# Optimization experiments

Hardware: AMD Instinct MI355X
Metric: run time of the kernel (lower is better)

The kernel has to match this reference:

```python
import jax, jax.numpy as jnp
import numpy as np

IN_F = 4096
OUT_F = 4096
RANK = 16
NUM_SLOTS = 32
ALPHA = 1.0


def setup_inputs() -> dict:
    key = jax.random.key(0)
    k_x, k_w, k_b, k_a, k_bm, k_idx = jax.random.split(key, 6)
    x = jax.random.normal(k_x, (8, 2048, IN_F), dtype=jnp.float32)
    weight = jax.random.normal(k_w, (OUT_F, IN_F), dtype=jnp.float32) * (1.0 / np.sqrt(IN_F))
    bias = jax.random.normal(k_b, (OUT_F,), dtype=jnp.float32) * 0.01
    lora_A = jax.random.normal(k_a, (NUM_SLOTS, IN_F, RANK), dtype=jnp.float32) * 1e-4
    lora_B = jax.random.normal(k_bm, (NUM_SLOTS, RANK, OUT_F), dtype=jnp.float32) * 1e-4
    lora_indices = jax.random.randint(k_idx, (8,), 0, NUM_SLOTS)
    return {"x": x, "weight": weight, "bias": bias, "lora_A": lora_A,
            "lora_B": lora_B, "lora_indices": lora_indices}


def reference(x, weight, bias, lora_A, lora_B, lora_indices):
    # base linear: x @ W.T + b
    out = jnp.einsum('bsd,od->bso', x, weight) + bias
    # per-sample LoRA slot gather + low-rank bmm chain
    chosen_A = lora_A[lora_indices]          # [B, in, r]
    chosen_B = lora_B[lora_indices]          # [B, r, out]
    inter = jnp.einsum('bsd,bdr->bsr', x, chosen_A)       # [B, S, r]
    out_lora = jnp.einsum('bsr,bro->bso', inter, chosen_B)  # [B, S, out]
    return out + ALPHA * out_lora
```

## Files before the change

### kernel.cpp

```cpp
#include <hip/hip_runtime.h>
#include <hip/hip_bf16.h>


#define M_TOT 16384
#define K_TOT 4096
#define N_TOT 4096
#define RANK 16
#define NT2 64

typedef __attribute__((ext_vector_type(8))) short bf16x8;
typedef __attribute__((ext_vector_type(4))) float f32x4;
typedef __attribute__((ext_vector_type(16))) float f32x16;

__device__ __forceinline__ unsigned short f2bf(float f) {
  unsigned int u = __builtin_bit_cast(unsigned int, f);
  u += 0x7fffu + ((u >> 16) & 1u);
  return (unsigned short)(u >> 16);
}

__global__ void cvt_bf16_kernel(const float* __restrict__ src,
                                unsigned short* __restrict__ dst, int n4) {
  int i = blockIdx.x * blockDim.x + threadIdx.x;
  const int stride = gridDim.x * blockDim.x;
  for (; i < n4; i += stride) {
    const float4 v = reinterpret_cast<const float4*>(src)[i];
    ushort4 o;
    o.x = f2bf(v.x); o.y = f2bf(v.y); o.z = f2bf(v.z); o.w = f2bf(v.w);
    reinterpret_cast<ushort4*>(dst)[i] = o;
  }
}

__global__ __launch_bounds__(256) void lora_inter_mfma_kernel(
    const unsigned short* __restrict__ xb,
    const float* __restrict__ loraA,
    const int* __restrict__ idx,
    float* __restrict__ inter) {
  const int lane = threadIdx.x & 63;
  const int wv = threadIdx.x >> 6;
  const int m0 = blockIdx.x * 64 + wv * 16;
  const int slot = idx[m0 >> 11];
  const int q = lane >> 4;
  const int c = lane & 15;
  const unsigned short* __restrict__ xrow = xb + (size_t)(m0 + c) * K_TOT + q * 8;
  const float* __restrict__ Abase = loraA + (size_t)slot * K_TOT * RANK + c;

  f32x4 acc = (f32x4){0.f, 0.f, 0.f, 0.f};
#pragma unroll 4
  for (int kt = 0; kt < K_TOT; kt += 32) {
    const bf16x8 af = *reinterpret_cast<const bf16x8*>(xrow + kt);
    const float* __restrict__ Ak = Abase + (size_t)(kt + q * 8) * RANK;
    bf16x8 bfr;
#pragma unroll
    for (int j = 0; j < 8; ++j) bfr[j] = (short)f2bf(Ak[(size_t)j * RANK]);
    acc = __builtin_amdgcn_mfma_f32_16x16x32_bf16(af, bfr, acc, 0, 0, 0);
  }
#pragma unroll
  for (int i = 0; i < 4; ++i)
    inter[(size_t)(m0 + q * 4 + i) * RANK + c] = acc[i];
}

__device__ __forceinline__ void gload16(const void* g, void* l) {
  __builtin_amdgcn_global_load_lds(
      (const __attribute__((address_space(1))) unsigned int*)g,
      (__attribute__((address_space(3))) unsigned int*)l, 16, 0, 0);
}

#define GBARRIER() asm volatile("s_barrier" ::: "memory")
#define RD(p) (*reinterpret_cast<const bf16x8*>(p))

__global__ __launch_bounds__(512, 2) void gemm_fused_kernel(
    const unsigned short* __restrict__ xb,
    const unsigned short* __restrict__ wb,
    const float* __restrict__ bias,
    const float* __restrict__ inter,
    const float* __restrict__ loraB,
    const int* __restrict__ idx,
    float* __restrict__ out) {
  __shared__ unsigned short lds[2][32768];
  char* ldsB = (char*)&lds[0][0];

  const int tid = threadIdx.x;
  const int lane = tid & 63;
  const int wv = tid >> 6;
  const int wr = wv >> 2;
  const int wc = wv & 3;

  const int bid = ((blockIdx.x & 7) << 7) | (blockIdx.x >> 3);
  const int m0 = (bid >> 4) << 8;
  const int n0 = (bid & 15) << 8;

  const int r0 = tid >> 3;
  const int scol = ((tid & 7) ^ (r0 & 7) ^ (((r0 >> 4) & 1) << 2)) << 3;
  const unsigned short* xsrc = xb + (size_t)(m0 + r0) * K_TOT + scol;
  const unsigned short* wsrc = wb + (size_t)(n0 + r0) * K_TOT + scol;
  const int stg = tid << 4;

#define STAGE64(t)                                                       \
  do {                                                                   \
    const int _bo = (((t) & 1) << 16);                                   \
    const size_t _ko = (size_t)(t) * 64;                                 \
    gload16(xsrc + _ko,                        ldsB + _bo + stg);        \
    gload16(xsrc + (size_t)64  * K_TOT + _ko,  ldsB + _bo + 8192 + stg); \
    gload16(xsrc + (size_t)128 * K_TOT + _ko,  ldsB + _bo + 16384 + stg);\
    gload16(xsrc + (size_t)192 * K_TOT + _ko,  ldsB + _bo + 24576 + stg);\
    gload16(wsrc + _ko,                        ldsB + _bo + 32768 + stg);\
    gload16(wsrc + (size_t)64  * K_TOT + _ko,  ldsB + _bo + 40960 + stg);\
    gload16(wsrc + (size_t)128 * K_TOT + _ko,  ldsB + _bo + 49152 + stg);\
    gload16(wsrc + (size_t)192 * K_TOT + _ko,  ldsB + _bo + 57344 + stg);\
  } while (0)

  const int rowl = lane & 31;
  const int hc = (((lane >> 5) ^ (lane & 7) ^ (((lane >> 4) & 1) << 2)) << 4);
  const int abase = (wr * 128 + rowl) * 128 + hc;
  const int bbase = 32768 + (wc * 64 + rowl) * 128 + hc;

  f32x16 acc[4][2];
#pragma unroll
  for (int i = 0; i < 4; ++i)
#pragma unroll
    for (int j = 0; j < 2; ++j)
#pragma unroll
      for (int e = 0; e < 16; ++e) acc[i][j][e] = 0.f;

  STAGE64(0);
  asm volatile("s_waitcnt vmcnt(0)" ::: "memory");
  GBARRIER();

#pragma unroll 1
  for (int t = 0; t < NT2; ++t) {
    const char* base = ldsB + ((t & 1) << 16);
    bf16x8 af[8], bf0[4], bf1[4];

#pragma unroll
    for (int ni = 0; ni < 2; ++ni)
#pragma unroll
      for (int kk = 0; kk < 2; ++kk)
        bf0[ni * 2 + kk] = RD(base + ((bbase + ni * 4096) ^ (kk << 5)));
#pragma unroll
    for (int mi = 0; mi < 4; ++mi)
#pragma unroll
      for (int kk = 0; kk < 2; ++kk)
        af[mi * 2 + kk] = RD(base + ((abase + mi * 4096) ^ (kk << 5)));
#pragma unroll
    for (int ni = 0; ni < 2; ++ni)
#pragma unroll
      for (int kk = 0; kk < 2; ++kk)
        bf1[ni * 2 + kk] = RD(base + ((bbase + ni * 4096) ^ ((2 + kk) << 5)));
    if (t < NT2 - 1) STAGE64(t + 1);

    asm volatile("s_waitcnt lgkmcnt(4)" ::: "memory");
    __builtin_amdgcn_sched_barrier(0);
    __builtin_amdgcn_s_setprio(1);
#pragma unroll
    for (int mi = 0; mi < 4; ++mi)
#pragma unroll
      for (int ni = 0; ni < 2; ++ni)
#pragma unroll
        for (int kk = 0; kk < 2; ++kk)
          acc[mi][ni] = __builtin_amdgcn_mfma_f32_32x32x16_bf16(
              af[mi * 2 + kk], bf0[ni * 2 + kk], acc[mi][ni], 0, 0, 0);
    __builtin_amdgcn_s_setprio(0);
    __builtin_amdgcn_sched_barrier(0);

#pragma unroll
    for (int mi = 0; mi < 4; ++mi)
#pragma unroll
      for (int kk = 0; kk < 2; ++kk)
        af[mi * 2 + kk] = RD(base + ((abase + mi * 4096) ^ ((2 + kk) << 5)));
    asm volatile("s_waitcnt lgkmcnt(0)" ::: "memory");
    __builtin_amdgcn_sched_barrier(0);
    __builtin_amdgcn_s_setprio(1);
#pragma unroll
    for (int mi = 0; mi < 4; ++mi)
#pragma unroll
      for (int ni = 0; ni < 2; ++ni)
#pragma unroll
        for (int kk = 0; kk < 2; ++kk)
          acc[mi][ni] = __builtin_amdgcn_mfma_f32_32x32x16_bf16(
              af[mi * 2 + kk], bf1[ni * 2 + kk], acc[mi][ni], 0, 0, 0);
    __builtin_amdgcn_s_setprio(0);
    __builtin_amdgcn_sched_barrier(0);

    asm volatile("s_waitcnt vmcnt(0)" ::: "memory");
    GBARRIER();
  }

  const int slot = idx[m0 >> 11];
  const float* __restrict__ Bmat = loraB + (size_t)slot * RANK * N_TOT;
  const int halfsel = (lane >> 5) << 2;
  const int gn0 = n0 + wc * 64 + rowl;

  float bcv[2][RANK];
  float bv[2];
#pragma unroll
  for (int ni = 0; ni < 2; ++ni) {
    const int gn = gn0 + ni * 32;
    bv[ni] = bias[gn];
#pragma unroll
    for (int p = 0; p < RANK; ++p) bcv[ni][p] = Bmat[(size_t)p * N_TOT + gn];
  }
#pragma unroll
  for (int mi = 0; mi < 4; ++mi) {
#pragma unroll
    for (int r = 0; r < 16; ++r) {
      const int gm = m0 + wr * 128 + mi * 32 + (r & 3) + 8 * (r >> 2) + halfsel;
      const float4* ivp = reinterpret_cast<const float4*>(inter + (size_t)gm * RANK);
      const float4 iv0 = ivp[0], iv1 = ivp[1], iv2 = ivp[2], iv3 = ivp[3];
      float* orow = out + (size_t)gm * N_TOT;
#pragma unroll
      for (int ni = 0; ni < 2; ++ni) {
        const float lora =
            iv0.x * bcv[ni][0]  + iv0.y * bcv[ni][1]  + iv0.z * bcv[ni][2]  + iv0.w * bcv[ni][3] +
            iv1.x * bcv[ni][4]  + iv1.y * bcv[ni][5]  + iv1.z * bcv[ni][6]  + iv1.w * bcv[ni][7] +
            iv2.x * bcv[ni][8]  + iv2.y * bcv[ni][9]  + iv2.z * bcv[ni][10] + iv2.w * bcv[ni][11] +
            iv3.x * bcv[ni][12] + iv3.y * bcv[ni][13] + iv3.z * bcv[ni][14] + iv3.w * bcv[ni][15];
        orow[gn0 + ni * 32] = acc[mi][ni][r] + bv[ni] + lora;
      }
    }
  }
#undef STAGE64
}

extern "C" void kernel_launch(void* const* d_in, const int* in_sizes, int n_in,
                              void* d_out, int out_size, void* d_ws, size_t ws_size,
                              hipStream_t stream) {
  const float* x     = (const float*)d_in[0];
  const float* w     = (const float*)d_in[1];
  const float* bias  = (const float*)d_in[2];
  const float* loraA = (const float*)d_in[3];
  const float* loraB = (const float*)d_in[4];
  const int*   idx   = (const int*)d_in[5];
  float* out = (float*)d_out;

  char* ws = (char*)d_ws;
  unsigned short* xb   = (unsigned short*)ws;
  unsigned short* wbuf = (unsigned short*)(ws + 134217728);
  float* inter = (float*)(ws + 134217728 + 33554432);

  cvt_bf16_kernel<<<2048, 256, 0, stream>>>(x, xb, M_TOT * K_TOT / 4);
  cvt_bf16_kernel<<<1024, 256, 0, stream>>>(w, wbuf, N_TOT * K_TOT / 4);
  lora_inter_mfma_kernel<<<M_TOT / 64, 256, 0, stream>>>(xb, loraA, idx, inter);
  gemm_fused_kernel<<<(M_TOT / 256) * (N_TOT / 256), 512, 0, stream>>>(
      xb, wbuf, bias, inter, loraB, idx, out);
}
```

Measured before the change: 718.9 us.

## Stage GEMM tiles in MFMA fragment order to make LDS reads linear

Reorganizes how global-to-LDS staging assigns rows and k-chunks so that each wavefront's 16-byte LDS slot already holds the fragment an MFMA lane needs. Fragment reads then become linear lane-contiguous addresses instead of XOR-swizzled ones, which removes swizzle arithmetic and aims at conflict-free ds_reads. The catch is that global loads become less coalesced: each lane fetches a 16-byte piece from a different row, and each thread now keeps eight separate source pointers in registers.

```diff
diff --git a/kernel.cpp b/kernel.cpp
--- a/kernel.cpp
+++ b/kernel.cpp
@@ -89,30 +89,37 @@
   const int m0 = (bid >> 4) << 8;
   const int n0 = (bid & 15) << 8;
 
-  const int r0 = tid >> 3;
-  const int scol = ((tid & 7) ^ (r0 & 7) ^ (((r0 >> 4) & 1) << 2)) << 3;
-  const unsigned short* xsrc = xb + (size_t)(m0 + r0) * K_TOT + scol;
-  const unsigned short* wsrc = wb + (size_t)(n0 + r0) * K_TOT + scol;
+  const unsigned short* asrc[4];
+  const unsigned short* bsrc[4];
+#pragma unroll
+  for (int j = 0; j < 4; ++j) {
+    const int fA = wv + 8 * j;
+    const int rowA = ((fA >> 4) & 1) * 128 + ((fA >> 2) & 3) * 32 + (lane & 31);
+    const int khA = (fA & 3) * 2 + (lane >> 5);
+    asrc[j] = xb + (size_t)(m0 + rowA) * K_TOT + khA * 8;
+    const int fB = wv + 8 * j;
+    const int rowB = (fB >> 3) * 64 + ((fB >> 2) & 1) * 32 + (lane & 31);
+    const int khB = (fB & 3) * 2 + (lane >> 5);
+    bsrc[j] = wb + (size_t)(n0 + rowB) * K_TOT + khB * 8;
+  }
   const int stg = tid << 4;
 
-#define STAGE64(t)                                                       \
-  do {                                                                   \
-    const int _bo = (((t) & 1) << 16);                                   \
-    const size_t _ko = (size_t)(t) * 64;                                 \
-    gload16(xsrc + _ko,                        ldsB + _bo + stg);        \
-    gload16(xsrc + (size_t)64  * K_TOT + _ko,  ldsB + _bo + 8192 + stg); \
-    gload16(xsrc + (size_t)128 * K_TOT + _ko,  ldsB + _bo + 16384 + stg);\
-    gload16(xsrc + (size_t)192 * K_TOT + _ko,  ldsB + _bo + 24576 + stg);\
-    gload16(wsrc + _ko,                        ldsB + _bo + 32768 + stg);\
-    gload16(wsrc + (size_t)64  * K_TOT + _ko,  ldsB + _bo + 40960 + stg);\
-    gload16(wsrc + (size_t)128 * K_TOT + _ko,  ldsB + _bo + 49152 + stg);\
-    gload16(wsrc + (size_t)192 * K_TOT + _ko,  ldsB + _bo + 57344 + stg);\
+#define STAGE64(t)                                                   \
+  do {                                                               \
+    const int _bo = (((t) & 1) << 16);                               \
+    const size_t _ko = (size_t)(t) * 64;                             \
+    gload16(asrc[0] + _ko, ldsB + _bo + stg);                        \
+    gload16(asrc[1] + _ko, ldsB + _bo + 8192 + stg);                 \
+    gload16(asrc[2] + _ko, ldsB + _bo + 16384 + stg);                \
+    gload16(asrc[3] + _ko, ldsB + _bo + 24576 + stg);                \
+    gload16(bsrc[0] + _ko, ldsB + _bo + 32768 + stg);                \
+    gload16(bsrc[1] + _ko, ldsB + _bo + 40960 + stg);                \
+    gload16(bsrc[2] + _ko, ldsB + _bo + 49152 + stg);                \
+    gload16(bsrc[3] + _ko, ldsB + _bo + 57344 + stg);                \
   } while (0)
 
-  const int rowl = lane & 31;
-  const int hc = (((lane >> 5) ^ (lane & 7) ^ (((lane >> 4) & 1) << 2)) << 4);
-  const int abase = (wr * 128 + rowl) * 128 + hc;
-  const int bbase = 32768 + (wc * 64 + rowl) * 128 + hc;
+  const int abase = (wr << 14) + (lane << 4);
+  const int bbase = 32768 + (wc << 13) + (lane << 4);
 
   f32x16 acc[4][2];
 #pragma unroll
@@ -135,17 +142,17 @@
     for (int ni = 0; ni < 2; ++ni)
 #pragma unroll
       for (int kk = 0; kk < 2; ++kk)
-        bf0[ni * 2 + kk] = RD(base + ((bbase + ni * 4096) ^ (kk << 5)));
-#pragma unroll
-    for (int mi = 0; mi < 4; ++mi)
-#pragma unroll
-      for (int kk = 0; kk < 2; ++kk)
-        af[mi * 2 + kk] = RD(base + ((abase + mi * 4096) ^ (kk << 5)));
+        bf0[ni * 2 + kk] = RD(base + bbase + ni * 4096 + kk * 1024);
+#pragma unroll
+    for (int mi = 0; mi < 4; ++mi)
+#pragma unroll
+      for (int kk = 0; kk < 2; ++kk)
+        af[mi * 2 + kk] = RD(base + abase + mi * 4096 + kk * 1024);
 #pragma unroll
     for (int ni = 0; ni < 2; ++ni)
 #pragma unroll
       for (int kk = 0; kk < 2; ++kk)
-        bf1[ni * 2 + kk] = RD(base + ((bbase + ni * 4096) ^ ((2 + kk) << 5)));
+        bf1[ni * 2 + kk] = RD(base + bbase + ni * 4096 + (2 + kk) * 1024);
     if (t < NT2 - 1) STAGE64(t + 1);
 
     asm volatile("s_waitcnt lgkmcnt(4)" ::: "memory");
@@ -166,7 +173,7 @@
     for (int mi = 0; mi < 4; ++mi)
 #pragma unroll
       for (int kk = 0; kk < 2; ++kk)
-        af[mi * 2 + kk] = RD(base + ((abase + mi * 4096) ^ ((2 + kk) << 5)));
+        af[mi * 2 + kk] = RD(base + abase + mi * 4096 + (2 + kk) * 1024);
     asm volatile("s_waitcnt lgkmcnt(0)" ::: "memory");
     __builtin_amdgcn_sched_barrier(0);
     __builtin_amdgcn_s_setprio(1);
@@ -187,6 +194,7 @@
 
   const int slot = idx[m0 >> 11];
   const float* __restrict__ Bmat = loraB + (size_t)slot * RANK * N_TOT;
+  const int rowl = lane & 31;
   const int halfsel = (lane >> 5) << 2;
   const int gn0 = n0 + wc * 64 + rowl;
 
```

Result: slower. 876.1 us (+21.9%).
